# Kernel tuning notes

Measured on AMD Instinct MI355X. Metric: run time of the kernel, lower is better.

The kernel has to match this reference:

```python
import jax, jax.numpy as jnp
import numpy as np
from jax import lax

MODES1, MODES2 = 16, 16
WIDTH = 64
T_IN, T_OUT = 10, 40
STATE, PAR = 1, 2
PAD = 9  # self.padding in FNO2d


def setup_inputs() -> dict:
    key = jax.random.key(0)
    ks = jax.random.split(key, 12)
    B, S = 32, 512
    u = jax.random.normal(ks[0], (B, S, T_IN), jnp.float32)
    x = jax.random.uniform(ks[1], (B, S), jnp.float32)
    t = jax.random.uniform(ks[2], (B, T_OUT), jnp.float32)
    par = jax.random.normal(ks[3], (B, PAR), jnp.float32)
    cin = T_IN + PAR + 2
    fc0_w = jax.random.normal(ks[4], (cin, WIDTH), jnp.float32) * 0.1
    fc0_b = jnp.zeros((WIDTH,), jnp.float32)
    scale = 1.0 / (WIDTH * WIDTH)
    spec_wr = jax.random.uniform(ks[5], (4, WIDTH, WIDTH, MODES1, MODES2), jnp.float32) * scale
    spec_wi = jax.random.uniform(ks[6], (4, WIDTH, WIDTH, MODES1, MODES2), jnp.float32) * scale
    w_conv = jax.random.normal(ks[7], (4, WIDTH, WIDTH), jnp.float32) * 0.05
    w_bias = jnp.zeros((4, WIDTH), jnp.float32)
    fc1_w = jax.random.normal(ks[8], (WIDTH, 128), jnp.float32) * 0.05
    fc1_b = jnp.zeros((128,), jnp.float32)
    fc2_w = jax.random.normal(ks[9], (128, STATE), jnp.float32) * 0.05
    fc2_b = jnp.zeros((STATE,), jnp.float32)
    return dict(u=u, x=x, t=t, par=par, fc0_w=fc0_w, fc0_b=fc0_b,
                spec_wr=spec_wr, spec_wi=spec_wi, w_conv=w_conv, w_bias=w_bias,
                fc1_w=fc1_w, fc1_b=fc1_b, fc2_w=fc2_w, fc2_b=fc2_b)


def _spectral_conv(v, wr, wi):
    # v: [B, Cin, X, T] real; wr/wi: [Cin, Cout, m1, m2]
    B, C, X, T = v.shape
    w = lax.complex(wr, wi)
    v_ft = jnp.fft.rfftn(v, axes=(2, 3))                      # [B, Cin, X, T//2+1] complex64
    corner = jnp.einsum('bixt,ioxt->boxt', v_ft[:, :, :MODES1, :MODES2], w)
    out_ft = jnp.zeros((B, w.shape[1], X, T // 2 + 1), jnp.complex64)
    out_ft = out_ft.at[:, :, :MODES1, :MODES2].set(corner)
    return jnp.fft.irfftn(out_ft, s=(X, T), axes=(2, 3))


def reference(u, x, t, par, fc0_w, fc0_b, spec_wr, spec_wi, w_conv, w_bias,
              fc1_w, fc1_b, fc2_w, fc2_b):
    B, S = u.shape[0], u.shape[1]
    # assemble (u repeated over T_out, par broadcast, grid (x, t)) -> [B,S,T_out,cin]
    uu = jnp.broadcast_to(u[:, :, None, :], (B, S, T_OUT, T_IN))
    pp = jnp.broadcast_to(par[:, None, None, :], (B, S, T_OUT, PAR))
    gx = jnp.broadcast_to(x[:, :, None, None], (B, S, T_OUT, 1))
    gt = jnp.broadcast_to(t[:, None, :, None], (B, S, T_OUT, 1))
    v = jnp.concatenate([uu, pp, gx, gt], axis=-1)
    v = v @ fc0_w + fc0_b                                      # [B,S,T_out,W]
    v = jnp.transpose(v, (0, 3, 1, 2))                         # [B,W,S,T_out]
    v = jnp.pad(v, ((0, 0), (0, 0), (0, PAD), (0, PAD)))       # pad right on x and t
    for i in range(4):
        u1 = _spectral_conv(v, spec_wr[i], spec_wi[i])
        u2 = jnp.einsum('bcxt,oc->boxt', v, w_conv[i]) + w_bias[i][None, :, None, None]
        v = u1 + u2
        if i < 3:
            v = jax.nn.gelu(v, approximate=False)
    v = v[:, :, :-PAD, :-PAD]
    v = jnp.transpose(v, (0, 2, 3, 1))                         # [B,S,T_out,W]
    v = jax.nn.gelu(v @ fc1_w + fc1_b, approximate=False)
    return v @ fc2_w + fc2_b                                   # [B,S,T_out,STATE]
```

## Files before the change

### kernel.cpp

```cpp
#include <hip/hip_runtime.h>
#include <math.h>

#define XDIM 521
#define TDIM 49
#define TPAD 52
#define XT (XDIM*TPAD)
#define NBTOT 32
#define NC 64
#define NS 512
#define NTO 40
#define NTIN 10
#define CIN 14
#define PI_D 3.14159265358979323846

__device__ __forceinline__ float gelu_f(float x){
  return 0.5f*x*(1.0f + erff(x*0.70710678118654752440f));
}

__global__ void k_init(float* __restrict__ TXC, float* __restrict__ TXS,
                       float* __restrict__ TTC, float* __restrict__ TTS,
                       float* __restrict__ ITC, float* __restrict__ ITS,
                       float* __restrict__ WT0, float* __restrict__ WT1, float* __restrict__ WTC,
                       const float* __restrict__ fc0_w, const float* __restrict__ fc1_w,
                       const float* __restrict__ w_conv){
  int i = blockIdx.x*256 + threadIdx.x;
  if (i < XDIM*16){
    int x = i >> 4, kx = i & 15;
    double ang = 2.0*PI_D*(double)((x*kx)%XDIM)/(double)XDIM;
    TXC[i] = (float)cos(ang);
    TXS[i] = (float)sin(ang);
  }
  if (i < TDIM*16){
    int t = i >> 4, kt = i & 15;
    double ang = 2.0*PI_D*(double)((t*kt)%TDIM)/(double)TDIM;
    TTC[i] = (float)cos(ang);
    TTS[i] = (float)sin(ang);
    double nrm = ((kt==0)?1.0:2.0)/(double)(XDIM*TDIM);
    ITC[i] = (float)(nrm*cos(ang));
    ITS[i] = (float)(nrm*sin(ang));
  }
  if (i < 64*16){
    int c = i >> 4, k = i & 15;
    WT0[i] = (k < CIN) ? fc0_w[k*64 + c] : 0.f;
  }
  if (i < 128*64){
    int j = i >> 6, c = i & 63;
    WT1[i] = fc1_w[c*128 + j];
  }
  if (i < 4*64*64){
    int l = i >> 12, r = i & 4095, c = r >> 6, o = r & 63;
    WTC[i] = w_conv[(l*64 + o)*64 + c];
  }
}

__global__ void k_fc0(const float* __restrict__ u, const float* __restrict__ xg,
                      const float* __restrict__ tg, const float* __restrict__ par,
                      const float* __restrict__ WT0, const float* __restrict__ fc0_b,
                      float* __restrict__ v, int b0){
  int bl = blockIdx.y;
  int b  = b0 + bl;
  int p = blockIdx.x*256 + threadIdx.x;
  if (p >= XT) return;
  int x = p / TPAD, t = p - x*TPAD;
  bool valid = (x < NS) && (t < NTO);
  float in[CIN];
  if (valid){
    #pragma unroll
    for (int k=0;k<NTIN;k++) in[k] = u[((size_t)(b*NS+x))*NTIN + k];
    in[10] = par[b*2+0]; in[11] = par[b*2+1];
    in[12] = xg[b*NS + x];
    in[13] = tg[b*NTO + t];
  } else {
    #pragma unroll
    for (int k=0;k<CIN;k++) in[k] = 0.f;
  }
  size_t base = ((size_t)bl*NC)*XT + p;
  for (int c=0;c<NC;c++){
    float acc = valid ? fc0_b[c] : 0.f;
    #pragma unroll
    for (int k=0;k<CIN;k++) acc = fmaf(in[k], WT0[c*16+k], acc);
    v[base + (size_t)c*XT] = acc;
  }
}

__device__ __forceinline__ void dft_reduce_emit(
    float (&ar)[16], float (&ai)[16], int w, int t,
    const float* __restrict__ TTC, const float* __restrict__ TTS,
    float* __restrict__ cVR, float* __restrict__ cVI, int bo, int NCB){
  __shared__ float redR[4*16*50], redI[4*16*50];
  if (t < TDIM){
    #pragma unroll
    for (int kx=0;kx<16;kx++){
      redR[(w*16+kx)*50 + t] = ar[kx];
      redI[(w*16+kx)*50 + t] = ai[kx];
    }
  }
  __syncthreads();
  int tid = w*64 + t;
  for (int q = tid; q < 784; q += 256){
    int kx = q/49, tt = q - kx*49;
    int idx = kx*50 + tt;
    float sR = redR[idx] + redR[800+idx] + redR[1600+idx] + redR[2400+idx];
    float sI = redI[idx] + redI[800+idx] + redI[1600+idx] + redI[2400+idx];
    redR[idx] = sR; redI[idx] = sI;
  }
  __syncthreads();
  int kx = tid >> 4, kt = tid & 15;
  float accR=0.f, accI=0.f;
  for (int tt=0; tt<TDIM; tt++){
    float vr = redR[kx*50+tt], vi = redI[kx*50+tt];
    float c = TTC[tt*16+kt], s = TTS[tt*16+kt];
    accR += vr*c + vi*s;
    accI += vi*c - vr*s;
  }
  cVR[(size_t)tid*NCB + bo] = accR;
  cVI[(size_t)tid*NCB + bo] = accI;
}

__global__ void __launch_bounds__(256) k_dftxt(const float* __restrict__ v,
    const float* __restrict__ TXC, const float* __restrict__ TXS,
    const float* __restrict__ TTC, const float* __restrict__ TTS,
    float* __restrict__ cVR, float* __restrict__ cVI, int NCB){
  int bo = blockIdx.x;
  int w = threadIdx.x >> 6, t = threadIdx.x & 63;
  bool act = (t < TDIM);
  const float* vp = v + (size_t)bo*XT + (act ? t : 0);
  float ar[16], ai[16];
  #pragma unroll
  for (int k=0;k<16;k++){ ar[k]=0.f; ai[k]=0.f; }
  if (w == 0){
    float v0 = act ? vp[0] : 0.f;
    #pragma unroll
    for (int k=0;k<16;k++) ar[k] += v0;
  }
  int p0 = 65*w + 1;
  #pragma unroll 2
  for (int p=p0; p<p0+65; p++){
    int xa = p, xb = XDIM - p;
    float va = act ? vp[xa*TPAD] : 0.f;
    float vbv= act ? vp[xb*TPAD] : 0.f;
    float sp = va + vbv, sm = va - vbv;
    const float4 tc0 = *reinterpret_cast<const float4*>(TXC + xa*16 + 0);
    const float4 tc1 = *reinterpret_cast<const float4*>(TXC + xa*16 + 4);
    const float4 tc2 = *reinterpret_cast<const float4*>(TXC + xa*16 + 8);
    const float4 tc3 = *reinterpret_cast<const float4*>(TXC + xa*16 + 12);
    const float4 ts0 = *reinterpret_cast<const float4*>(TXS + xa*16 + 0);
    const float4 ts1 = *reinterpret_cast<const float4*>(TXS + xa*16 + 4);
    const float4 ts2 = *reinterpret_cast<const float4*>(TXS + xa*16 + 8);
    const float4 ts3 = *reinterpret_cast<const float4*>(TXS + xa*16 + 12);
    ar[0]  = fmaf(sp, tc0.x, ar[0]);  ai[0]  = fmaf(-sm, ts0.x, ai[0]);
    ar[1]  = fmaf(sp, tc0.y, ar[1]);  ai[1]  = fmaf(-sm, ts0.y, ai[1]);
    ar[2]  = fmaf(sp, tc0.z, ar[2]);  ai[2]  = fmaf(-sm, ts0.z, ai[2]);
    ar[3]  = fmaf(sp, tc0.w, ar[3]);  ai[3]  = fmaf(-sm, ts0.w, ai[3]);
    ar[4]  = fmaf(sp, tc1.x, ar[4]);  ai[4]  = fmaf(-sm, ts1.x, ai[4]);
    ar[5]  = fmaf(sp, tc1.y, ar[5]);  ai[5]  = fmaf(-sm, ts1.y, ai[5]);
    ar[6]  = fmaf(sp, tc1.z, ar[6]);  ai[6]  = fmaf(-sm, ts1.z, ai[6]);
    ar[7]  = fmaf(sp, tc1.w, ar[7]);  ai[7]  = fmaf(-sm, ts1.w, ai[7]);
    ar[8]  = fmaf(sp, tc2.x, ar[8]);  ai[8]  = fmaf(-sm, ts2.x, ai[8]);
    ar[9]  = fmaf(sp, tc2.y, ar[9]);  ai[9]  = fmaf(-sm, ts2.y, ai[9]);
    ar[10] = fmaf(sp, tc2.z, ar[10]); ai[10] = fmaf(-sm, ts2.z, ai[10]);
    ar[11] = fmaf(sp, tc2.w, ar[11]); ai[11] = fmaf(-sm, ts2.w, ai[11]);
    ar[12] = fmaf(sp, tc3.x, ar[12]); ai[12] = fmaf(-sm, ts3.x, ai[12]);
    ar[13] = fmaf(sp, tc3.y, ar[13]); ai[13] = fmaf(-sm, ts3.y, ai[13]);
    ar[14] = fmaf(sp, tc3.z, ar[14]); ai[14] = fmaf(-sm, ts3.z, ai[14]);
    ar[15] = fmaf(sp, tc3.w, ar[15]); ai[15] = fmaf(-sm, ts3.w, ai[15]);
  }
  dft_reduce_emit(ar, ai, w, t, TTC, TTS, cVR, cVI, bo, NCB);
}

__global__ void k_spec(const float* __restrict__ swr, const float* __restrict__ swi,
                       const float* __restrict__ cVR, const float* __restrict__ cVI,
                       float* __restrict__ cOR, float* __restrict__ cOI, int l, int NCB){
  int m = blockIdx.x;
  __shared__ float wr[4096], wi[4096];
  __shared__ float vr[32*65], vi[32*65];
  const size_t wb = (size_t)l*64*64*256 + m;
  for (int q = threadIdx.x; q < 4096; q += 256){
    wr[q] = swr[wb + (size_t)q*256];
    wi[q] = swi[wb + (size_t)q*256];
  }
  for (int q = threadIdx.x; q < NCB; q += 256){
    int b=q>>6, i=q&63;
    vr[b*65+i] = cVR[(size_t)m*NCB+q];
    vi[b*65+i] = cVI[(size_t)m*NCB+q];
  }
  __syncthreads();
  int b = threadIdx.x >> 3, og = threadIdx.x & 7;
  if (b*64 < NCB){
    float oR[8], oI[8];
    #pragma unroll
    for (int j=0;j<8;j++){ oR[j]=0.f; oI[j]=0.f; }
    for (int i=0;i<64;i++){
      float arv = vr[b*65+i], aiv = vi[b*65+i];
      #pragma unroll
      for (int j=0;j<8;j++){
        float wrv = wr[i*64 + og*8 + j], wiv = wi[i*64 + og*8 + j];
        oR[j] = fmaf(arv,wrv,fmaf(-aiv,wiv,oR[j]));
        oI[j] = fmaf(arv,wiv,fmaf( aiv,wrv,oI[j]));
      }
    }
    #pragma unroll
    for (int j=0;j<8;j++){
      cOR[(size_t)m*NCB + b*64 + og*8 + j] = oR[j];
      cOI[(size_t)m*NCB + b*64 + og*8 + j] = oI[j];
    }
  }
}

__global__ void __launch_bounds__(256) k_invG(const float* __restrict__ cOR, const float* __restrict__ cOI,
    const float* __restrict__ ITC, const float* __restrict__ ITS,
    float* __restrict__ GR, float* __restrict__ GI, int NCB){
  int bo = blockIdx.x;
  __shared__ float lcr[256], lci[256];
  int q = threadIdx.x;
  lcr[q] = cOR[(size_t)q*NCB + bo];
  lci[q] = cOI[(size_t)q*NCB + bo];
  __syncthreads();
  int kx = q >> 4, tq = q & 15;
  for (int t = tq; t < TDIM; t += 16){
    float gr=0.f, gi=0.f;
    #pragma unroll
    for (int kt=0;kt<16;kt++){
      float cr = lcr[kx*16+kt], ci = lci[kx*16+kt];
      float wc = ITC[t*16+kt], ws = ITS[t*16+kt];
      gr = fmaf(cr,wc,fmaf(-ci,ws,gr));
      gi = fmaf(cr,ws,fmaf( ci,wc,gi));
    }
    GR[(size_t)bo*784 + kx*TDIM + t] = gr;
    GI[(size_t)bo*784 + kx*TDIM + t] = gi;
  }
}

__global__ void __launch_bounds__(256) k_conv(float* __restrict__ v,
    const float* __restrict__ WTC, const float* __restrict__ w_bias, int l){
  int bl = blockIdx.y;
  int p = blockIdx.x*512 + threadIdx.x*2;
  if (p >= XT) return;
  const float* wl = WTC + l*4096;
  float a0[64], a1[64];
  #pragma unroll
  for (int o=0;o<64;o++){ a0[o]=0.f; a1[o]=0.f; }
  const size_t bb = (size_t)bl*NC*XT;
  for (int c=0;c<NC;c++){
    const float2 vv = *reinterpret_cast<const float2*>(v + bb + (size_t)c*XT + p);
    #pragma unroll
    for (int o=0;o<64;o++){
      float wv = wl[c*64+o];
      a0[o] = fmaf(vv.x, wv, a0[o]);
      a1[o] = fmaf(vv.y, wv, a1[o]);
    }
  }
  #pragma unroll
  for (int o=0;o<64;o++){
    float bias = w_bias[l*64+o];
    float2 rr; rr.x = a0[o]+bias; rr.y = a1[o]+bias;
    *reinterpret_cast<float2*>(v + bb + (size_t)o*XT + p) = rr;
  }
}

template<int GELU, int EMIT>
__global__ void __launch_bounds__(256) k_inv2dft(const float* __restrict__ GR, const float* __restrict__ GI,
    const float* __restrict__ TXC, const float* __restrict__ TXS,
    const float* __restrict__ TTC, const float* __restrict__ TTS,
    float* __restrict__ v, float* __restrict__ cVR, float* __restrict__ cVI, int NCB){
  int bo = blockIdx.x;
  int w = threadIdx.x >> 6, t = threadIdx.x & 63;
  bool act = (t < TDIM);
  int tcl = act ? t : 0;
  float gr[16], gi[16];
  #pragma unroll
  for (int kx=0;kx<16;kx++){
    gr[kx] = GR[(size_t)bo*784 + kx*TDIM + tcl];
    gi[kx] = GI[(size_t)bo*784 + kx*TDIM + tcl];
  }
  float ar[16], ai[16];
  #pragma unroll
  for (int k=0;k<16;k++){ ar[k]=0.f; ai[k]=0.f; }
  float* vb = v + (size_t)bo*XT;
  if (w == 0){
    float s1 = 0.f;
    #pragma unroll
    for (int k=0;k<16;k++) s1 += gr[k];
    float r = 0.f;
    if (act){
      r = s1 + vb[t];
      if (GELU) r = gelu_f(r);
    }
    if (t < TPAD) vb[t] = r;
    if (EMIT){
      #pragma unroll
      for (int k=0;k<16;k++) ar[k] += r;
    }
  }
  int p0 = 65*w + 1;
  #pragma unroll 2
  for (int p=p0; p<p0+65; p++){
    int xa = p, xb = XDIM - p;
    const float4 tc0 = *reinterpret_cast<const float4*>(TXC + xa*16 + 0);
    const float4 tc1 = *reinterpret_cast<const float4*>(TXC + xa*16 + 4);
    const float4 tc2 = *reinterpret_cast<const float4*>(TXC + xa*16 + 8);
    const float4 tc3 = *reinterpret_cast<const float4*>(TXC + xa*16 + 12);
    const float4 ts0 = *reinterpret_cast<const float4*>(TXS + xa*16 + 0);
    const float4 ts1 = *reinterpret_cast<const float4*>(TXS + xa*16 + 4);
    const float4 ts2 = *reinterpret_cast<const float4*>(TXS + xa*16 + 8);
    const float4 ts3 = *reinterpret_cast<const float4*>(TXS + xa*16 + 12);
    float s1, s2;
    s1  = gr[0]*tc0.x;             s2  = gi[0]*ts0.x;
    s1  = fmaf(gr[1],  tc0.y, s1); s2  = fmaf(gi[1],  ts0.y, s2);
    s1  = fmaf(gr[2],  tc0.z, s1); s2  = fmaf(gi[2],  ts0.z, s2);
    s1  = fmaf(gr[3],  tc0.w, s1); s2  = fmaf(gi[3],  ts0.w, s2);
    s1  = fmaf(gr[4],  tc1.x, s1); s2  = fmaf(gi[4],  ts1.x, s2);
    s1  = fmaf(gr[5],  tc1.y, s1); s2  = fmaf(gi[5],  ts1.y, s2);
    s1  = fmaf(gr[6],  tc1.z, s1); s2  = fmaf(gi[6],  ts1.z, s2);
    s1  = fmaf(gr[7],  tc1.w, s1); s2  = fmaf(gi[7],  ts1.w, s2);
    s1  = fmaf(gr[8],  tc2.x, s1); s2  = fmaf(gi[8],  ts2.x, s2);
    s1  = fmaf(gr[9],  tc2.y, s1); s2  = fmaf(gi[9],  ts2.y, s2);
    s1  = fmaf(gr[10], tc2.z, s1); s2  = fmaf(gi[10], ts2.z, s2);
    s1  = fmaf(gr[11], tc2.w, s1); s2  = fmaf(gi[11], ts2.w, s2);
    s1  = fmaf(gr[12], tc3.x, s1); s2  = fmaf(gi[12], ts3.x, s2);
    s1  = fmaf(gr[13], tc3.y, s1); s2  = fmaf(gi[13], ts3.y, s2);
    s1  = fmaf(gr[14], tc3.z, s1); s2  = fmaf(gi[14], ts3.z, s2);
    s1  = fmaf(gr[15], tc3.w, s1); s2  = fmaf(gi[15], ts3.w, s2);
    float accA = s1 - s2, accB = s1 + s2;
    float rA = 0.f, rB = 0.f;
    if (act){
      rA = accA + vb[(size_t)xa*TPAD + t];
      rB = accB + vb[(size_t)xb*TPAD + t];
      if (GELU){ rA = gelu_f(rA); rB = gelu_f(rB); }
    }
    if (t < TPAD){
      vb[(size_t)xa*TPAD + t] = rA;
      vb[(size_t)xb*TPAD + t] = rB;
    }
    if (EMIT){
      float sp = rA + rB, sm = rA - rB;
      ar[0]  = fmaf(sp, tc0.x, ar[0]);  ai[0]  = fmaf(-sm, ts0.x, ai[0]);
      ar[1]  = fmaf(sp, tc0.y, ar[1]);  ai[1]  = fmaf(-sm, ts0.y, ai[1]);
      ar[2]  = fmaf(sp, tc0.z, ar[2]);  ai[2]  = fmaf(-sm, ts0.z, ai[2]);
      ar[3]  = fmaf(sp, tc0.w, ar[3]);  ai[3]  = fmaf(-sm, ts0.w, ai[3]);
      ar[4]  = fmaf(sp, tc1.x, ar[4]);  ai[4]  = fmaf(-sm, ts1.x, ai[4]);
      ar[5]  = fmaf(sp, tc1.y, ar[5]);  ai[5]  = fmaf(-sm, ts1.y, ai[5]);
      ar[6]  = fmaf(sp, tc1.z, ar[6]);  ai[6]  = fmaf(-sm, ts1.z, ai[6]);
      ar[7]  = fmaf(sp, tc1.w, ar[7]);  ai[7]  = fmaf(-sm, ts1.w, ai[7]);
      ar[8]  = fmaf(sp, tc2.x, ar[8]);  ai[8]  = fmaf(-sm, ts2.x, ai[8]);
      ar[9]  = fmaf(sp, tc2.y, ar[9]);  ai[9]  = fmaf(-sm, ts2.y, ai[9]);
      ar[10] = fmaf(sp, tc2.z, ar[10]); ai[10] = fmaf(-sm, ts2.z, ai[10]);
      ar[11] = fmaf(sp, tc2.w, ar[11]); ai[11] = fmaf(-sm, ts2.w, ai[11]);
      ar[12] = fmaf(sp, tc3.x, ar[12]); ai[12] = fmaf(-sm, ts3.x, ai[12]);
      ar[13] = fmaf(sp, tc3.y, ar[13]); ai[13] = fmaf(-sm, ts3.y, ai[13]);
      ar[14] = fmaf(sp, tc3.z, ar[14]); ai[14] = fmaf(-sm, ts3.z, ai[14]);
      ar[15] = fmaf(sp, tc3.w, ar[15]); ai[15] = fmaf(-sm, ts3.w, ai[15]);
    }
  }
  if (EMIT) dft_reduce_emit(ar, ai, w, t, TTC, TTS, cVR, cVI, bo, NCB);
}

__global__ void k_final(const float* __restrict__ v, const float* __restrict__ WT1,
                        const float* __restrict__ fc1_b, const float* __restrict__ fc2_w,
                        const float* __restrict__ fc2_b, float* __restrict__ out, int b0){
  int bl = blockIdx.y;
  int pp = blockIdx.x*256 + threadIdx.x;
  int s = pp / NTO, to = pp - s*NTO;
  float vr[64];
  size_t vb = (size_t)bl*NC*XT + (size_t)s*TPAD + to;
  #pragma unroll
  for (int c=0;c<64;c++) vr[c] = v[vb + (size_t)c*XT];
  float acc = fc2_b[0];
  for (int j=0;j<128;j++){
    float h = fc1_b[j];
    #pragma unroll
    for (int c=0;c<64;c++) h = fmaf(vr[c], WT1[j*64+c], h);
    h = gelu_f(h);
    acc = fmaf(h, fc2_w[j], acc);
  }
  out[((size_t)(b0+bl))*20480 + pp] = acc;
}

extern "C" void kernel_launch(void* const* d_in, const int* in_sizes, int n_in,
                              void* d_out, int out_size, void* d_ws, size_t ws_size,
                              hipStream_t stream){
  const float* u     = (const float*)d_in[0];
  const float* xg    = (const float*)d_in[1];
  const float* tg    = (const float*)d_in[2];
  const float* par   = (const float*)d_in[3];
  const float* fc0_w = (const float*)d_in[4];
  const float* fc0_b = (const float*)d_in[5];
  const float* swr   = (const float*)d_in[6];
  const float* swi   = (const float*)d_in[7];
  const float* wconv = (const float*)d_in[8];
  const float* wbias = (const float*)d_in[9];
  const float* fc1_w = (const float*)d_in[10];
  const float* fc1_b = (const float*)d_in[11];
  const float* fc2_w = (const float*)d_in[12];
  const float* fc2_b = (const float*)d_in[13];

  int nb = NBTOT;
  while (nb > 1){
    size_t need = (45408ull + (size_t)nb*64ull*29684ull) * 4ull;
    if (need <= ws_size) break;
    nb >>= 1;
  }
  const int NCB = nb*64;

  float* W = (float*)d_ws;
  size_t off = 0;
  float* TXC = W + off; off += 8336;
  float* TXS = W + off; off += 8336;
  float* TTC = W + off; off += 784;
  float* TTS = W + off; off += 784;
  float* ITC = W + off; off += 784;
  float* ITS = W + off; off += 784;
  float* WT0 = W + off; off += 1024;
  float* WT1 = W + off; off += 8192;
  float* WTC = W + off; off += 16384;
  float* VA  = W + off; off += (size_t)NCB*XT;
  float* VXR = W + off; off += (size_t)NCB*784;
  float* VXI = W + off; off += (size_t)NCB*784;
  float* CVR = W + off; off += (size_t)256*NCB;
  float* CVI = W + off; off += (size_t)256*NCB;
  float* COR = W + off; off += (size_t)256*NCB;
  float* COI = W + off; off += (size_t)256*NCB;

  k_init<<<64, 256, 0, stream>>>(TXC,TXS,TTC,TTS,ITC,ITS,WT0,WT1,WTC, fc0_w, fc1_w, wconv);

  const int nch = NBTOT / nb;
  for (int ch = 0; ch < nch; ch++){
    int b0 = ch*nb;
    k_fc0<<<dim3((XT+255)/256, nb), 256, 0, stream>>>(u, xg, tg, par, WT0, fc0_b, VA, b0);
    k_dftxt<<<NCB, 256, 0, stream>>>(VA, TXC, TXS, TTC, TTS, CVR, CVI, NCB);
    for (int l=0; l<4; l++){
      k_spec<<<256, 256, 0, stream>>>(swr, swi, CVR, CVI, COR, COI, l, NCB);
      k_invG<<<NCB, 256, 0, stream>>>(COR, COI, ITC, ITS, VXR, VXI, NCB);
      k_conv<<<dim3(53, nb), 256, 0, stream>>>(VA, WTC, wbias, l);
      if (l < 3) k_inv2dft<1,1><<<NCB, 256, 0, stream>>>(VXR, VXI, TXC, TXS, TTC, TTS, VA, CVR, CVI, NCB);
      else       k_inv2dft<0,0><<<NCB, 256, 0, stream>>>(VXR, VXI, TXC, TXS, TTC, TTS, VA, CVR, CVI, NCB);
    }
    k_final<<<dim3(80, nb), 256, 0, stream>>>(VA, WT1, fc1_b, fc2_w, fc2_b, (float*)d_out, b0);
  }
}
```

Measured before the change: 1.944 ms.

## Split forward and inverse DFT kernels across two blocks per channel

The k_dftxt and k_inv2dft kernels now launch two blocks per (batch, channel) slice. Each block covers half of the x-range, in chunks of roughly 32 rows per wave instead of 65. The two partial spectral sums go to separate buffers, with the second reusing COR/COI, and k_spec adds them when it loads its input. This aims to raise block count and occupancy on the DFT stages. In exchange it adds an extra global read in k_spec, drops the unroll-2 pragma, and aliases the second partial buffer with k_spec's output, violating its __restrict__ assumptions.

Result: faster. 1.818 ms (-6.5%).

```diff
diff --git a/kernel.cpp b/kernel.cpp
--- a/kernel.cpp
+++ b/kernel.cpp
@@ -120,22 +120,23 @@
 __global__ void __launch_bounds__(256) k_dftxt(const float* __restrict__ v,
     const float* __restrict__ TXC, const float* __restrict__ TXS,
     const float* __restrict__ TTC, const float* __restrict__ TTS,
-    float* __restrict__ cVR, float* __restrict__ cVI, int NCB){
-  int bo = blockIdx.x;
+    float* __restrict__ cVR0, float* __restrict__ cVI0,
+    float* __restrict__ cVR1, float* __restrict__ cVI1, int NCB){
+  int bo = blockIdx.x >> 1, h = blockIdx.x & 1;
   int w = threadIdx.x >> 6, t = threadIdx.x & 63;
   bool act = (t < TDIM);
   const float* vp = v + (size_t)bo*XT + (act ? t : 0);
   float ar[16], ai[16];
   #pragma unroll
   for (int k=0;k<16;k++){ ar[k]=0.f; ai[k]=0.f; }
-  if (w == 0){
+  if (h == 0 && w == 0){
     float v0 = act ? vp[0] : 0.f;
     #pragma unroll
     for (int k=0;k<16;k++) ar[k] += v0;
   }
-  int p0 = 65*w + 1;
-  #pragma unroll 2
-  for (int p=p0; p<p0+65; p++){
+  int chunk = h*4 + w;
+  int p0 = 1 + (chunk*65)/2, p1 = 1 + ((chunk+1)*65)/2;
+  for (int p=p0; p<p1; p++){
     int xa = p, xb = XDIM - p;
     float va = act ? vp[xa*TPAD] : 0.f;
     float vbv= act ? vp[xb*TPAD] : 0.f;
@@ -165,11 +166,12 @@
     ar[14] = fmaf(sp, tc3.z, ar[14]); ai[14] = fmaf(-sm, ts3.z, ai[14]);
     ar[15] = fmaf(sp, tc3.w, ar[15]); ai[15] = fmaf(-sm, ts3.w, ai[15]);
   }
-  dft_reduce_emit(ar, ai, w, t, TTC, TTS, cVR, cVI, bo, NCB);
+  dft_reduce_emit(ar, ai, w, t, TTC, TTS, h ? cVR1 : cVR0, h ? cVI1 : cVI0, bo, NCB);
 }
 
 __global__ void k_spec(const float* __restrict__ swr, const float* __restrict__ swi,
-                       const float* __restrict__ cVR, const float* __restrict__ cVI,
+                       const float* __restrict__ cVR0, const float* __restrict__ cVI0,
+                       const float* __restrict__ cVR1, const float* __restrict__ cVI1,
                        float* __restrict__ cOR, float* __restrict__ cOI, int l, int NCB){
   int m = blockIdx.x;
   __shared__ float wr[4096], wi[4096];
@@ -181,8 +183,8 @@
   }
   for (int q = threadIdx.x; q < NCB; q += 256){
     int b=q>>6, i=q&63;
-    vr[b*65+i] = cVR[(size_t)m*NCB+q];
-    vi[b*65+i] = cVI[(size_t)m*NCB+q];
+    vr[b*65+i] = cVR0[(size_t)m*NCB+q] + cVR1[(size_t)m*NCB+q];
+    vi[b*65+i] = cVI0[(size_t)m*NCB+q] + cVI1[(size_t)m*NCB+q];
   }
   __syncthreads();
   int b = threadIdx.x >> 3, og = threadIdx.x & 7;
@@ -262,8 +264,10 @@
 __global__ void __launch_bounds__(256) k_inv2dft(const float* __restrict__ GR, const float* __restrict__ GI,
     const float* __restrict__ TXC, const float* __restrict__ TXS,
     const float* __restrict__ TTC, const float* __restrict__ TTS,
-    float* __restrict__ v, float* __restrict__ cVR, float* __restrict__ cVI, int NCB){
-  int bo = blockIdx.x;
+    float* __restrict__ v,
+    float* __restrict__ cVR0, float* __restrict__ cVI0,
+    float* __restrict__ cVR1, float* __restrict__ cVI1, int NCB){
+  int bo = blockIdx.x >> 1, h = blockIdx.x & 1;
   int w = threadIdx.x >> 6, t = threadIdx.x & 63;
   bool act = (t < TDIM);
   int tcl = act ? t : 0;
@@ -277,7 +281,7 @@
   #pragma unroll
   for (int k=0;k<16;k++){ ar[k]=0.f; ai[k]=0.f; }
   float* vb = v + (size_t)bo*XT;
-  if (w == 0){
+  if (h == 0 && w == 0){
     float s1 = 0.f;
     #pragma unroll
     for (int k=0;k<16;k++) s1 += gr[k];
@@ -292,9 +296,9 @@
       for (int k=0;k<16;k++) ar[k] += r;
     }
   }
-  int p0 = 65*w + 1;
-  #pragma unroll 2
-  for (int p=p0; p<p0+65; p++){
+  int chunk = h*4 + w;
+  int p0 = 1 + (chunk*65)/2, p1 = 1 + ((chunk+1)*65)/2;
+  for (int p=p0; p<p1; p++){
     int xa = p, xb = XDIM - p;
     const float4 tc0 = *reinterpret_cast<const float4*>(TXC + xa*16 + 0);
     const float4 tc1 = *reinterpret_cast<const float4*>(TXC + xa*16 + 4);
@@ -352,7 +356,7 @@
       ar[15] = fmaf(sp, tc3.w, ar[15]); ai[15] = fmaf(-sm, ts3.w, ai[15]);
     }
   }
-  if (EMIT) dft_reduce_emit(ar, ai, w, t, TTC, TTS, cVR, cVI, bo, NCB);
+  if (EMIT) dft_reduce_emit(ar, ai, w, t, TTC, TTS, h ? cVR1 : cVR0, h ? cVI1 : cVI0, bo, NCB);
 }
 
 __global__ void k_final(const float* __restrict__ v, const float* __restrict__ WT1,
@@ -427,13 +431,13 @@
   for (int ch = 0; ch < nch; ch++){
     int b0 = ch*nb;
     k_fc0<<<dim3((XT+255)/256, nb), 256, 0, stream>>>(u, xg, tg, par, WT0, fc0_b, VA, b0);
-    k_dftxt<<<NCB, 256, 0, stream>>>(VA, TXC, TXS, TTC, TTS, CVR, CVI, NCB);
+    k_dftxt<<<NCB*2, 256, 0, stream>>>(VA, TXC, TXS, TTC, TTS, CVR, CVI, COR, COI, NCB);
     for (int l=0; l<4; l++){
-      k_spec<<<256, 256, 0, stream>>>(swr, swi, CVR, CVI, COR, COI, l, NCB);
+      k_spec<<<256, 256, 0, stream>>>(swr, swi, CVR, CVI, COR, COI, COR, COI, l, NCB);
       k_invG<<<NCB, 256, 0, stream>>>(COR, COI, ITC, ITS, VXR, VXI, NCB);
       k_conv<<<dim3(53, nb), 256, 0, stream>>>(VA, WTC, wbias, l);
-      if (l < 3) k_inv2dft<1,1><<<NCB, 256, 0, stream>>>(VXR, VXI, TXC, TXS, TTC, TTS, VA, CVR, CVI, NCB);
-      else       k_inv2dft<0,0><<<NCB, 256, 0, stream>>>(VXR, VXI, TXC, TXS, TTC, TTS, VA, CVR, CVI, NCB);
+      if (l < 3) k_inv2dft<1,1><<<NCB*2, 256, 0, stream>>>(VXR, VXI, TXC, TXS, TTC, TTS, VA, CVR, CVI, COR, COI, NCB);
+      else       k_inv2dft<0,0><<<NCB*2, 256, 0, stream>>>(VXR, VXI, TXC, TXS, TTC, TTS, VA, CVR, CVI, COR, COI, NCB);
     }
     k_final<<<dim3(80, nb), 256, 0, stream>>>(VA, WT1, fc1_b, fc2_w, fc2_b, (float*)d_out, b0);
   }
```
